# Performance work log

Measured on AMD Instinct MI355X. Metric: run time of the kernel, lower is better.

The kernel has to match this reference:

```python
import jax, jax.numpy as jnp
import numpy as np

C = 256
CK = C // 8  # query/key channels = 32


def setup_inputs() -> dict:
    key = jax.random.key(0)
    ks = jax.random.split(key, 7)
    sc = 0.05
    x = jax.random.normal(ks[0], (4, C, 64, 64), dtype=jnp.float32)
    Wq = jax.random.normal(ks[1], (CK, C), dtype=jnp.float32) * sc
    bq = jax.random.normal(ks[2], (CK,), dtype=jnp.float32) * sc
    Wk = jax.random.normal(ks[3], (CK, C), dtype=jnp.float32) * sc
    bk = jax.random.normal(ks[4], (CK,), dtype=jnp.float32) * sc
    Wv = jax.random.normal(ks[5], (C, C), dtype=jnp.float32) * sc
    bv = jax.random.normal(ks[6], (C,), dtype=jnp.float32) * sc
    gamma = jnp.array([0.5], dtype=jnp.float32)  # nonzero so output/grads are nontrivial
    return {"x": x, "Wq": Wq, "bq": bq, "Wk": Wk, "bk": bk, "Wv": Wv, "bv": bv, "gamma": gamma}


def reference(x, Wq, bq, Wk, bk, Wv, bv, gamma):
    B, Cc, H, W = x.shape
    xf = x.reshape(B, Cc, H * W)  # [B, C, N]
    # 1x1 conv1d == channel-wise matmul
    f = jnp.einsum('kc,bcn->bkn', Wq, xf) + bq[None, :, None]  # [B, CK, N]
    g = jnp.einsum('kc,bcn->bkn', Wk, xf) + bk[None, :, None]  # [B, CK, N]
    h = jnp.einsum('oc,bcn->bon', Wv, xf) + bv[None, :, None]  # [B, C, N]
    # unscaled attention scores: s[b,i,j] = sum_k f[b,k,i] g[b,k,j]
    s = jnp.einsum('bki,bkj->bij', f, g)  # [B, N, N]
    beta = jax.nn.softmax(s, axis=1)      # softmax over query-side axis i (dim=1)
    o = jnp.einsum('bci,bij->bcj', h, beta)  # [B, C, N]
    o = gamma[0] * o
    return o.reshape(B, Cc, H, W)
```

## Files before the change

kernel.cpp:

```cpp
#include <hip/hip_runtime.h>
#include <math.h>

#define BB 4
#define CC 256
#define CKK 32
#define NN 4096
#define TI 32
#define NT (NN / TI)
#define SM_OFF 40.0f

typedef __attribute__((ext_vector_type(8))) short short8v;
typedef __attribute__((ext_vector_type(4))) short short4v;
typedef __attribute__((ext_vector_type(4))) float f32x4;

static __device__ inline unsigned short f2bf(float x) {
    union { float f; unsigned u; } v; v.f = x;
    unsigned r = v.u + 0x7fffu + ((v.u >> 16) & 1u);
    return (unsigned short)(r >> 16);
}
static __device__ inline float bf2f(unsigned short h) {
    union { unsigned u; float f; } v; v.u = ((unsigned)h) << 16;
    return v.f;
}

__global__ __launch_bounds__(256) void prep_w(
    const float* __restrict__ Wq, const float* __restrict__ Wk,
    const float* __restrict__ Wv, unsigned short* __restrict__ Wbf)
{
    int e = blockIdx.x * 256 + threadIdx.x;
    int row = e >> 8, c = e & 255;
    float v;
    if (row < 32)      v = Wq[row * 256 + c];
    else if (row < 64) v = Wk[(row - 32) * 256 + c];
    else               v = Wv[(row - 64) * 256 + c];
    Wbf[e] = f2bf(v);
}

__global__ __launch_bounds__(256, 4) void proj_kernel(
    const float* __restrict__ x,
    const unsigned short* __restrict__ Wbf,
    const float* __restrict__ bq, const float* __restrict__ bk,
    const float* __restrict__ bv,
    unsigned short* __restrict__ fF, unsigned short* __restrict__ gT,
    unsigned short* __restrict__ hF)
{
    __shared__ unsigned short xsh[32 * 264];
    __shared__ unsigned short xsl[32 * 264];

    const int t = threadIdx.x;
    const int b = blockIdx.x >> 7;
    const int n_b = (blockIdx.x & 127) * 32;
    const int lane = t & 63;
    const int wave = t >> 6;
    const int jl = lane & 15;
    const int quad = lane >> 4;

    {
        const int q = t & 7, cb = t >> 3;
        #pragma unroll
        for (int cc = 0; cc < 8; ++cc) {
            int c = cb + cc * 32;
            float4 v = *(const float4*)(x + ((size_t)b * CC + c) * NN + n_b + q * 4);
            float vv[4] = {v.x, v.y, v.z, v.w};
            #pragma unroll
            for (int e = 0; e < 4; ++e) {
                int n = q * 4 + e;
                unsigned short h = f2bf(vv[e]);
                unsigned short l = f2bf(vv[e] - bf2f(h));
                xsh[n * 264 + c] = h;
                xsl[n * 264 + c] = l;
            }
        }
    }
    __syncthreads();

    const int rowbase_w = wave * 80;
    #pragma unroll 1
    for (int nt = 0; nt < 2; ++nt) {
        short8v bhi[8], blo[8];
        #pragma unroll
        for (int k = 0; k < 8; ++k) {
            bhi[k] = *(const short8v*)&xsh[(nt * 16 + jl) * 264 + k * 32 + quad * 8];
            blo[k] = *(const short8v*)&xsl[(nt * 16 + jl) * 264 + k * 32 + quad * 8];
        }
        const int ng = n_b + nt * 16 + jl;
        const int it  = ng >> 5;
        const int il  = ng & 31;
        const int ihh = (ng >> 4) & 1;
        #pragma unroll 1
        for (int mt = 0; mt < 5; ++mt) {
            int rowbase = rowbase_w + mt * 16;
            const unsigned short* wrow = Wbf + (size_t)(rowbase + jl) * CC;
            f32x4 acch = (f32x4){0.f, 0.f, 0.f, 0.f};
            f32x4 accl = (f32x4){0.f, 0.f, 0.f, 0.f};
            #pragma unroll
            for (int k = 0; k < 8; ++k) {
                short8v a = *(const short8v*)(wrow + k * 32 + quad * 8);
                acch = __builtin_amdgcn_mfma_f32_16x16x32_bf16(a, bhi[k], acch, 0, 0, 0);
                accl = __builtin_amdgcn_mfma_f32_16x16x32_bf16(a, blo[k], accl, 0, 0, 0);
            }
            f32x4 acc;
            #pragma unroll
            for (int r = 0; r < 4; ++r) acc[r] = acch[r] + accl[r];
            int rlo = rowbase + quad * 4;
            if (rowbase < 32) {
                float4 bias = *(const float4*)(bq + rlo);
                short4v o;
                o[0] = (short)f2bf(acc[0] + bias.x); o[1] = (short)f2bf(acc[1] + bias.y);
                o[2] = (short)f2bf(acc[2] + bias.z); o[3] = (short)f2bf(acc[3] + bias.w);
                size_t dst = (((size_t)b * NT + it) * 2 + ihh) * 512
                           + (size_t)((rlo >> 3) * 16 + (ng & 15)) * 8 + (rlo & 7);
                *(short4v*)(fF + dst) = o;
            } else if (rowbase < 64) {
                float4 bias = *(const float4*)(bk + rlo - 32);
                short4v o;
                o[0] = (short)f2bf(acc[0] + bias.x); o[1] = (short)f2bf(acc[1] + bias.y);
                o[2] = (short)f2bf(acc[2] + bias.z); o[3] = (short)f2bf(acc[3] + bias.w);
                *(short4v*)(gT + ((size_t)b * NN + ng) * CKK + (rlo - 32)) = o;
            } else {
                const float* bp = bv + rlo - 64;
                #pragma unroll
                for (int r = 0; r < 4; ++r) {
                    int c = rlo - 64 + r;
                    size_t dst = (((size_t)b * NT + it) * 16 + (c >> 4)) * 512
                               + (size_t)((il >> 3) * 16 + (c & 15)) * 8 + (il & 7);
                    hF[dst] = f2bf(acc[r] + bp[r]);
                }
            }
        }
    }
}

__global__ __launch_bounds__(512, 2) void attn_kernel(
    const unsigned short* __restrict__ fF,
    const unsigned short* __restrict__ gT,
    const unsigned short* __restrict__ hF,
    const float* __restrict__ gamma,
    float* __restrict__ out)
{
    __shared__ unsigned short pa[2][4][512];
    __shared__ float ls[8][16];
    __shared__ float ls2[4][16];

    const int t = threadIdx.x;
    const int lane = t & 63;
    const int wave = t >> 6;
    const int bi = blockIdx.x;
    const int b  = bi & 3;
    const int j0 = (bi >> 2) * 64;
    const int jl = lane & 15;
    const int quad = lane >> 4;
    const int jc = wave & 3;
    const int ih = wave >> 2;
    const int c0 = wave * 32;
    const int cg0 = wave * 2;

    const unsigned short* fFb = fF + (size_t)b * NT * 2 * 512;
    const unsigned short* hFb = hF + (size_t)b * NT * 16 * 512;

    short8v bg = *(const short8v*)(gT + ((size_t)b * NN + j0 + jc * 16 + jl) * CKK + quad * 8);

    f32x4 acc[8];
    #pragma unroll
    for (int q = 0; q < 8; ++q) acc[q] = (f32x4){0.f, 0.f, 0.f, 0.f};
    float l_run = 0.f;

    const f32x4 zoff = (f32x4){-SM_OFF, -SM_OFF, -SM_OFF, -SM_OFF};

    const int Lw = ((ih * 2 + (quad >> 1)) * 16 + jl) * 8 + (quad & 1) * 4;

    short8v af0 = *(const short8v*)(fFb + (size_t)(0 * 2 + ih) * 512 + lane * 8);
    short8v ahc0 = *(const short8v*)(hFb + ((size_t)0 * 16 + cg0 + 0) * 512 + lane * 8);
    short8v ahc1 = *(const short8v*)(hFb + ((size_t)0 * 16 + cg0 + 1) * 512 + lane * 8);
    f32x4 s0 = __builtin_amdgcn_mfma_f32_16x16x32_bf16(af0, bg, zoff, 0, 0, 0);
    short8v afn = *(const short8v*)(fFb + (size_t)(1 * 2 + ih) * 512 + lane * 8);
    {
        float e0 = __expf(s0[0]), e1 = __expf(s0[1]);
        float e2 = __expf(s0[2]), e3 = __expf(s0[3]);
        l_run += (e0 + e1) + (e2 + e3);
        unsigned p01, p23;
        asm("v_cvt_pk_bf16_f32 %0, %1, %2" : "=v"(p01) : "v"(e0), "v"(e1));
        asm("v_cvt_pk_bf16_f32 %0, %1, %2" : "=v"(p23) : "v"(e2), "v"(e3));
        uint2 pw; pw.x = p01; pw.y = p23;
        *(uint2*)&pa[0][jc][Lw] = pw;
    }
    asm volatile("s_waitcnt lgkmcnt(0)" ::: "memory");
    __builtin_amdgcn_s_barrier();
    asm volatile("" ::: "memory");

    #pragma unroll 1
    for (int it = 0; it < NT - 1; ++it) {
        const int buf = it & 1;

        f32x4 s = __builtin_amdgcn_mfma_f32_16x16x32_bf16(afn, bg, zoff, 0, 0, 0);

        {
            const int i2 = (it + 2 < NT ? it + 2 : NT - 1);
            afn = *(const short8v*)(fFb + ((size_t)i2 * 2 + ih) * 512 + lane * 8);
        }
        short8v ahn0 = *(const short8v*)(hFb + ((size_t)(it + 1) * 16 + cg0 + 0) * 512 + lane * 8);
        short8v ahn1 = *(const short8v*)(hFb + ((size_t)(it + 1) * 16 + cg0 + 1) * 512 + lane * 8);

        #pragma unroll
        for (int jc2 = 0; jc2 < 4; ++jc2) {
            short8v bp = *(const short8v*)&pa[buf][jc2][lane * 8];
            acc[jc2 * 2 + 0] = __builtin_amdgcn_mfma_f32_16x16x32_bf16(ahc0, bp, acc[jc2 * 2 + 0], 0, 0, 0);
            acc[jc2 * 2 + 1] = __builtin_amdgcn_mfma_f32_16x16x32_bf16(ahc1, bp, acc[jc2 * 2 + 1], 0, 0, 0);
        }

        {
            float e0 = __expf(s[0]), e1 = __expf(s[1]);
            float e2 = __expf(s[2]), e3 = __expf(s[3]);
            l_run += (e0 + e1) + (e2 + e3);
            unsigned p01, p23;
            asm("v_cvt_pk_bf16_f32 %0, %1, %2" : "=v"(p01) : "v"(e0), "v"(e1));
            asm("v_cvt_pk_bf16_f32 %0, %1, %2" : "=v"(p23) : "v"(e2), "v"(e3));
            uint2 pw; pw.x = p01; pw.y = p23;
            *(uint2*)&pa[buf ^ 1][jc][Lw] = pw;
        }

        asm volatile("s_waitcnt lgkmcnt(0)" ::: "memory");
        __builtin_amdgcn_s_barrier();
        asm volatile("" ::: "memory");

        ahc0 = ahn0; ahc1 = ahn1;
    }

    {
        const int buf = (NT - 1) & 1;
        #pragma unroll
        for (int jc2 = 0; jc2 < 4; ++jc2) {
            short8v bp = *(const short8v*)&pa[buf][jc2][lane * 8];
            acc[jc2 * 2 + 0] = __builtin_amdgcn_mfma_f32_16x16x32_bf16(ahc0, bp, acc[jc2 * 2 + 0], 0, 0, 0);
            acc[jc2 * 2 + 1] = __builtin_amdgcn_mfma_f32_16x16x32_bf16(ahc1, bp, acc[jc2 * 2 + 1], 0, 0, 0);
        }
    }

    l_run += __shfl_xor(l_run, 16, 64);
    l_run += __shfl_xor(l_run, 32, 64);
    if (quad == 0) ls[wave][jl] = l_run;
    __syncthreads();
    if (wave < 4 && quad == 0)
        ls2[wave][jl] = gamma[0] / (ls[wave][jl] + ls[wave + 4][jl]);
    __syncthreads();

    #pragma unroll
    for (int jc2 = 0; jc2 < 4; ++jc2) {
        float sc = ls2[jc2][jl];
        #pragma unroll
        for (int cc = 0; cc < 2; ++cc) {
            f32x4 a = acc[jc2 * 2 + cc];
            size_t addr = ((size_t)b * CC + c0 + cc * 16 + quad * 4) * NN + j0 + jc2 * 16 + jl;
            #pragma unroll
            for (int r = 0; r < 4; ++r)
                out[addr + (size_t)r * NN] = a[r] * sc;
        }
    }
}

extern "C" void kernel_launch(void* const* d_in, const int* in_sizes, int n_in,
                              void* d_out, int out_size, void* d_ws, size_t ws_size,
                              hipStream_t stream) {
    const float* x     = (const float*)d_in[0];
    const float* Wq    = (const float*)d_in[1];
    const float* bq    = (const float*)d_in[2];
    const float* Wk    = (const float*)d_in[3];
    const float* bk    = (const float*)d_in[4];
    const float* Wv    = (const float*)d_in[5];
    const float* bv    = (const float*)d_in[6];
    const float* gamma = (const float*)d_in[7];
    float* out = (float*)d_out;

    unsigned short* Wbf = (unsigned short*)d_ws;
    unsigned short* fF  = Wbf + 320 * 256;
    unsigned short* gT  = fF + (size_t)BB * NN * CKK;
    unsigned short* hF  = gT + (size_t)BB * NN * CKK;

    prep_w<<<320, 256, 0, stream>>>(Wq, Wk, Wv, Wbf);
    proj_kernel<<<BB * (NN / 32), 256, 0, stream>>>(x, Wbf, bq, bk, bv, fF, gT, hF);
    attn_kernel<<<BB * (NN / 64), 512, 0, stream>>>(fF, gT, hF, gamma, out);
}
```

Measured before the change: 159.8 us.

## Split PV accumulation by alternating i-tiles across wave halves with LDS reduction

Each wave now owns 64 output channels instead of 32 and handles only every other i-tile for the P·V MFMA, alternating between the two wave halves. Each wave therefore loads four h fragments every other iteration instead of two every iteration. The two partial accumulators are summed through a new LDS buffer before output. Compute-heavy iterations are raised with s_setprio so one half's MFMA work can overlap the other half's exp and softmax work, at the cost of doubled accumulator registers and extra LDS use, which may lower occupancy.

```diff
diff --git a/kernel.cpp b/kernel.cpp
--- a/kernel.cpp
+++ b/kernel.cpp
@@ -139,6 +139,7 @@
     float* __restrict__ out)
 {
     __shared__ unsigned short pa[2][4][512];
+    __shared__ f32x4 eb[4][4][4][64];
     __shared__ float ls[8][16];
     __shared__ float ls2[4][16];
 
@@ -150,30 +151,30 @@
     const int j0 = (bi >> 2) * 64;
     const int jl = lane & 15;
     const int quad = lane >> 4;
-    const int jc = wave & 3;
-    const int ih = wave >> 2;
-    const int c0 = wave * 32;
-    const int cg0 = wave * 2;
+    const int cg  = wave & 3;
+    const int ihw = wave >> 2;
 
     const unsigned short* fFb = fF + (size_t)b * NT * 2 * 512;
     const unsigned short* hFb = hF + (size_t)b * NT * 16 * 512;
 
-    short8v bg = *(const short8v*)(gT + ((size_t)b * NN + j0 + jc * 16 + jl) * CKK + quad * 8);
-
-    f32x4 acc[8];
+    short8v bg = *(const short8v*)(gT + ((size_t)b * NN + j0 + cg * 16 + jl) * CKK + quad * 8);
+
+    f32x4 acc[16];
     #pragma unroll
-    for (int q = 0; q < 8; ++q) acc[q] = (f32x4){0.f, 0.f, 0.f, 0.f};
+    for (int q = 0; q < 16; ++q) acc[q] = (f32x4){0.f, 0.f, 0.f, 0.f};
     float l_run = 0.f;
 
     const f32x4 zoff = (f32x4){-SM_OFF, -SM_OFF, -SM_OFF, -SM_OFF};
 
-    const int Lw = ((ih * 2 + (quad >> 1)) * 16 + jl) * 8 + (quad & 1) * 4;
-
-    short8v af0 = *(const short8v*)(fFb + (size_t)(0 * 2 + ih) * 512 + lane * 8);
-    short8v ahc0 = *(const short8v*)(hFb + ((size_t)0 * 16 + cg0 + 0) * 512 + lane * 8);
-    short8v ahc1 = *(const short8v*)(hFb + ((size_t)0 * 16 + cg0 + 1) * 512 + lane * 8);
+    const int Lw = ((ihw * 2 + (quad >> 1)) * 16 + jl) * 8 + (quad & 1) * 4;
+
+    short8v af0 = *(const short8v*)(fFb + (size_t)(0 * 2 + ihw) * 512 + lane * 8);
+    short8v ah0 = *(const short8v*)(hFb + ((size_t)ihw * 16 + cg * 4 + 0) * 512 + lane * 8);
+    short8v ah1 = *(const short8v*)(hFb + ((size_t)ihw * 16 + cg * 4 + 1) * 512 + lane * 8);
+    short8v ah2 = *(const short8v*)(hFb + ((size_t)ihw * 16 + cg * 4 + 2) * 512 + lane * 8);
+    short8v ah3 = *(const short8v*)(hFb + ((size_t)ihw * 16 + cg * 4 + 3) * 512 + lane * 8);
     f32x4 s0 = __builtin_amdgcn_mfma_f32_16x16x32_bf16(af0, bg, zoff, 0, 0, 0);
-    short8v afn = *(const short8v*)(fFb + (size_t)(1 * 2 + ih) * 512 + lane * 8);
+    short8v afn = *(const short8v*)(fFb + (size_t)(1 * 2 + ihw) * 512 + lane * 8);
     {
         float e0 = __expf(s0[0]), e1 = __expf(s0[1]);
         float e2 = __expf(s0[2]), e3 = __expf(s0[3]);
@@ -182,7 +183,7 @@
         asm("v_cvt_pk_bf16_f32 %0, %1, %2" : "=v"(p01) : "v"(e0), "v"(e1));
         asm("v_cvt_pk_bf16_f32 %0, %1, %2" : "=v"(p23) : "v"(e2), "v"(e3));
         uint2 pw; pw.x = p01; pw.y = p23;
-        *(uint2*)&pa[0][jc][Lw] = pw;
+        *(uint2*)&pa[0][cg][Lw] = pw;
     }
     asm volatile("s_waitcnt lgkmcnt(0)" ::: "memory");
     __builtin_amdgcn_s_barrier();
@@ -193,19 +194,30 @@
         const int buf = it & 1;
 
         f32x4 s = __builtin_amdgcn_mfma_f32_16x16x32_bf16(afn, bg, zoff, 0, 0, 0);
-
         {
-            const int i2 = (it + 2 < NT ? it + 2 : NT - 1);
-            afn = *(const short8v*)(fFb + ((size_t)i2 * 2 + ih) * 512 + lane * 8);
-        }
-        short8v ahn0 = *(const short8v*)(hFb + ((size_t)(it + 1) * 16 + cg0 + 0) * 512 + lane * 8);
-        short8v ahn1 = *(const short8v*)(hFb + ((size_t)(it + 1) * 16 + cg0 + 1) * 512 + lane * 8);
-
-        #pragma unroll
-        for (int jc2 = 0; jc2 < 4; ++jc2) {
-            short8v bp = *(const short8v*)&pa[buf][jc2][lane * 8];
-            acc[jc2 * 2 + 0] = __builtin_amdgcn_mfma_f32_16x16x32_bf16(ahc0, bp, acc[jc2 * 2 + 0], 0, 0, 0);
-            acc[jc2 * 2 + 1] = __builtin_amdgcn_mfma_f32_16x16x32_bf16(ahc1, bp, acc[jc2 * 2 + 1], 0, 0, 0);
+            const int i2f = (it + 2 < NT ? it + 2 : NT - 1);
+            afn = *(const short8v*)(fFb + ((size_t)i2f * 2 + ihw) * 512 + lane * 8);
+        }
+
+        const bool on = ((it & 1) == ihw);
+        short8v an0, an1, an2, an3;
+        if (on) {
+            const int i2 = (it + 2 <= NT - 2 + ihw) ? it + 2 : it;
+            an0 = *(const short8v*)(hFb + ((size_t)i2 * 16 + cg * 4 + 0) * 512 + lane * 8);
+            an1 = *(const short8v*)(hFb + ((size_t)i2 * 16 + cg * 4 + 1) * 512 + lane * 8);
+            an2 = *(const short8v*)(hFb + ((size_t)i2 * 16 + cg * 4 + 2) * 512 + lane * 8);
+            an3 = *(const short8v*)(hFb + ((size_t)i2 * 16 + cg * 4 + 3) * 512 + lane * 8);
+
+            __builtin_amdgcn_s_setprio(1);
+            #pragma unroll
+            for (int jc2 = 0; jc2 < 4; ++jc2) {
+                short8v bp = *(const short8v*)&pa[buf][jc2][lane * 8];
+                acc[jc2 * 4 + 0] = __builtin_amdgcn_mfma_f32_16x16x32_bf16(ah0, bp, acc[jc2 * 4 + 0], 0, 0, 0);
+                acc[jc2 * 4 + 1] = __builtin_amdgcn_mfma_f32_16x16x32_bf16(ah1, bp, acc[jc2 * 4 + 1], 0, 0, 0);
+                acc[jc2 * 4 + 2] = __builtin_amdgcn_mfma_f32_16x16x32_bf16(ah2, bp, acc[jc2 * 4 + 2], 0, 0, 0);
+                acc[jc2 * 4 + 3] = __builtin_amdgcn_mfma_f32_16x16x32_bf16(ah3, bp, acc[jc2 * 4 + 3], 0, 0, 0);
+            }
+            __builtin_amdgcn_s_setprio(0);
         }
 
         {
@@ -216,41 +228,53 @@
             asm("v_cvt_pk_bf16_f32 %0, %1, %2" : "=v"(p01) : "v"(e0), "v"(e1));
             asm("v_cvt_pk_bf16_f32 %0, %1, %2" : "=v"(p23) : "v"(e2), "v"(e3));
             uint2 pw; pw.x = p01; pw.y = p23;
-            *(uint2*)&pa[buf ^ 1][jc][Lw] = pw;
+            *(uint2*)&pa[buf ^ 1][cg][Lw] = pw;
         }
 
         asm volatile("s_waitcnt lgkmcnt(0)" ::: "memory");
         __builtin_amdgcn_s_barrier();
         asm volatile("" ::: "memory");
 
-        ahc0 = ahn0; ahc1 = ahn1;
-    }
-
-    {
+        if (on) { ah0 = an0; ah1 = an1; ah2 = an2; ah3 = an3; }
+    }
+
+    if (ihw == 1) {
         const int buf = (NT - 1) & 1;
         #pragma unroll
         for (int jc2 = 0; jc2 < 4; ++jc2) {
             short8v bp = *(const short8v*)&pa[buf][jc2][lane * 8];
-            acc[jc2 * 2 + 0] = __builtin_amdgcn_mfma_f32_16x16x32_bf16(ahc0, bp, acc[jc2 * 2 + 0], 0, 0, 0);
-            acc[jc2 * 2 + 1] = __builtin_amdgcn_mfma_f32_16x16x32_bf16(ahc1, bp, acc[jc2 * 2 + 1], 0, 0, 0);
+            acc[jc2 * 4 + 0] = __builtin_amdgcn_mfma_f32_16x16x32_bf16(ah0, bp, acc[jc2 * 4 + 0], 0, 0, 0);
+            acc[jc2 * 4 + 1] = __builtin_amdgcn_mfma_f32_16x16x32_bf16(ah1, bp, acc[jc2 * 4 + 1], 0, 0, 0);
+            acc[jc2 * 4 + 2] = __builtin_amdgcn_mfma_f32_16x16x32_bf16(ah2, bp, acc[jc2 * 4 + 2], 0, 0, 0);
+            acc[jc2 * 4 + 3] = __builtin_amdgcn_mfma_f32_16x16x32_bf16(ah3, bp, acc[jc2 * 4 + 3], 0, 0, 0);
         }
     }
 
     l_run += __shfl_xor(l_run, 16, 64);
     l_run += __shfl_xor(l_run, 32, 64);
     if (quad == 0) ls[wave][jl] = l_run;
+
+    const int jw = (1 - ihw) * 2;
+    #pragma unroll
+    for (int m = 0; m < 2; ++m)
+        #pragma unroll
+        for (int cc = 0; cc < 4; ++cc)
+            eb[cg][jw + m][cc][lane] = acc[(jw + m) * 4 + cc];
     __syncthreads();
+
     if (wave < 4 && quad == 0)
         ls2[wave][jl] = gamma[0] / (ls[wave][jl] + ls[wave + 4][jl]);
     __syncthreads();
 
+    const int jr = ihw * 2;
     #pragma unroll
-    for (int jc2 = 0; jc2 < 4; ++jc2) {
+    for (int m = 0; m < 2; ++m) {
+        const int jc2 = jr + m;
         float sc = ls2[jc2][jl];
         #pragma unroll
-        for (int cc = 0; cc < 2; ++cc) {
-            f32x4 a = acc[jc2 * 2 + cc];
-            size_t addr = ((size_t)b * CC + c0 + cc * 16 + quad * 4) * NN + j0 + jc2 * 16 + jl;
+        for (int cc = 0; cc < 4; ++cc) {
+            f32x4 a = acc[jc2 * 4 + cc] + eb[cg][jc2][cc][lane];
+            size_t addr = ((size_t)b * CC + cg * 64 + cc * 16 + quad * 4) * NN + j0 + jc2 * 16 + jl;
             #pragma unroll
             for (int r = 0; r < 4; ++r)
                 out[addr + (size_t)r * NN] = a[r] * sc;
```

New measurement: 324.1 us. 2.03x slower.

## Process two query tiles per barrier iteration and raise MFMA wave priority

Applied to the files above, without the earlier changes.

The attention main loop now handles two 32-row query tiles per iteration, with a doubled shared-memory P buffer. This halves the number of block-wide barriers and deepens prefetch of f and h fragments. The PV MFMA section is also wrapped in s_setprio to favour matrix work over the exp phase of other waves. In exchange, register pressure and LDS use go up, which could hurt occupancy at 2 blocks per CU.

```diff
diff --git a/kernel.cpp b/kernel.cpp
--- a/kernel.cpp
+++ b/kernel.cpp
@@ -138,7 +138,7 @@
     const float* __restrict__ gamma,
     float* __restrict__ out)
 {
-    __shared__ unsigned short pa[2][4][512];
+    __shared__ unsigned short pa[2][2][4][512];
     __shared__ float ls[8][16];
     __shared__ float ls2[4][16];
 
@@ -152,7 +152,6 @@
     const int quad = lane >> 4;
     const int jc = wave & 3;
     const int ih = wave >> 2;
-    const int c0 = wave * 32;
     const int cg0 = wave * 2;
 
     const unsigned short* fFb = fF + (size_t)b * NT * 2 * 512;
@@ -169,70 +168,107 @@
 
     const int Lw = ((ih * 2 + (quad >> 1)) * 16 + jl) * 8 + (quad & 1) * 4;
 
-    short8v af0 = *(const short8v*)(fFb + (size_t)(0 * 2 + ih) * 512 + lane * 8);
-    short8v ahc0 = *(const short8v*)(hFb + ((size_t)0 * 16 + cg0 + 0) * 512 + lane * 8);
-    short8v ahc1 = *(const short8v*)(hFb + ((size_t)0 * 16 + cg0 + 1) * 512 + lane * 8);
-    f32x4 s0 = __builtin_amdgcn_mfma_f32_16x16x32_bf16(af0, bg, zoff, 0, 0, 0);
-    short8v afn = *(const short8v*)(fFb + (size_t)(1 * 2 + ih) * 512 + lane * 8);
+    short8v afA = *(const short8v*)(fFb + (size_t)(0 * 2 + ih) * 512 + lane * 8);
+    short8v afB = *(const short8v*)(fFb + (size_t)(1 * 2 + ih) * 512 + lane * 8);
+    short8v ahA0 = *(const short8v*)(hFb + ((size_t)0 * 16 + cg0 + 0) * 512 + lane * 8);
+    short8v ahA1 = *(const short8v*)(hFb + ((size_t)0 * 16 + cg0 + 1) * 512 + lane * 8);
+    short8v ahB0 = *(const short8v*)(hFb + ((size_t)1 * 16 + cg0 + 0) * 512 + lane * 8);
+    short8v ahB1 = *(const short8v*)(hFb + ((size_t)1 * 16 + cg0 + 1) * 512 + lane * 8);
+    f32x4 s0A = __builtin_amdgcn_mfma_f32_16x16x32_bf16(afA, bg, zoff, 0, 0, 0);
+    f32x4 s0B = __builtin_amdgcn_mfma_f32_16x16x32_bf16(afB, bg, zoff, 0, 0, 0);
+    afA = *(const short8v*)(fFb + (size_t)(2 * 2 + ih) * 512 + lane * 8);
+    afB = *(const short8v*)(fFb + (size_t)(3 * 2 + ih) * 512 + lane * 8);
     {
-        float e0 = __expf(s0[0]), e1 = __expf(s0[1]);
-        float e2 = __expf(s0[2]), e3 = __expf(s0[3]);
-        l_run += (e0 + e1) + (e2 + e3);
-        unsigned p01, p23;
+        float e0 = __expf(s0A[0]), e1 = __expf(s0A[1]);
+        float e2 = __expf(s0A[2]), e3 = __expf(s0A[3]);
+        float f0 = __expf(s0B[0]), f1 = __expf(s0B[1]);
+        float f2 = __expf(s0B[2]), f3 = __expf(s0B[3]);
+        l_run += ((e0 + e1) + (e2 + e3)) + ((f0 + f1) + (f2 + f3));
+        unsigned p01, p23, q01, q23;
         asm("v_cvt_pk_bf16_f32 %0, %1, %2" : "=v"(p01) : "v"(e0), "v"(e1));
         asm("v_cvt_pk_bf16_f32 %0, %1, %2" : "=v"(p23) : "v"(e2), "v"(e3));
+        asm("v_cvt_pk_bf16_f32 %0, %1, %2" : "=v"(q01) : "v"(f0), "v"(f1));
+        asm("v_cvt_pk_bf16_f32 %0, %1, %2" : "=v"(q23) : "v"(f2), "v"(f3));
         uint2 pw; pw.x = p01; pw.y = p23;
-        *(uint2*)&pa[0][jc][Lw] = pw;
+        uint2 qw; qw.x = q01; qw.y = q23;
+        *(uint2*)&pa[0][0][jc][Lw] = pw;
+        *(uint2*)&pa[0][1][jc][Lw] = qw;
     }
     asm volatile("s_waitcnt lgkmcnt(0)" ::: "memory");
     __builtin_amdgcn_s_barrier();
     asm volatile("" ::: "memory");
 
     #pragma unroll 1
-    for (int it = 0; it < NT - 1; ++it) {
-        const int buf = it & 1;
-
-        f32x4 s = __builtin_amdgcn_mfma_f32_16x16x32_bf16(afn, bg, zoff, 0, 0, 0);
+    for (int it2 = 0; it2 < NT / 2 - 1; ++it2) {
+        const int buf = it2 & 1;
+        const int tn = 2 * it2 + 2;
+
+        f32x4 sA = __builtin_amdgcn_mfma_f32_16x16x32_bf16(afA, bg, zoff, 0, 0, 0);
+        f32x4 sB = __builtin_amdgcn_mfma_f32_16x16x32_bf16(afB, bg, zoff, 0, 0, 0);
 
         {
-            const int i2 = (it + 2 < NT ? it + 2 : NT - 1);
-            afn = *(const short8v*)(fFb + ((size_t)i2 * 2 + ih) * 512 + lane * 8);
-        }
-        short8v ahn0 = *(const short8v*)(hFb + ((size_t)(it + 1) * 16 + cg0 + 0) * 512 + lane * 8);
-        short8v ahn1 = *(const short8v*)(hFb + ((size_t)(it + 1) * 16 + cg0 + 1) * 512 + lane * 8);
-
+            const int i4 = (tn + 2 < NT ? tn + 2 : NT - 1);
+            const int i5 = (tn + 3 < NT ? tn + 3 : NT - 1);
+            afA = *(const short8v*)(fFb + ((size_t)i4 * 2 + ih) * 512 + lane * 8);
+            afB = *(const short8v*)(fFb + ((size_t)i5 * 2 + ih) * 512 + lane * 8);
+        }
+        short8v anA0 = *(const short8v*)(hFb + ((size_t)tn * 16 + cg0 + 0) * 512 + lane * 8);
+        short8v anA1 = *(const short8v*)(hFb + ((size_t)tn * 16 + cg0 + 1) * 512 + lane * 8);
+        short8v anB0 = *(const short8v*)(hFb + ((size_t)(tn + 1) * 16 + cg0 + 0) * 512 + lane * 8);
+        short8v anB1 = *(const short8v*)(hFb + ((size_t)(tn + 1) * 16 + cg0 + 1) * 512 + lane * 8);
+
+        __builtin_amdgcn_s_setprio(1);
         #pragma unroll
         for (int jc2 = 0; jc2 < 4; ++jc2) {
-            short8v bp = *(const short8v*)&pa[buf][jc2][lane * 8];
-            acc[jc2 * 2 + 0] = __builtin_amdgcn_mfma_f32_16x16x32_bf16(ahc0, bp, acc[jc2 * 2 + 0], 0, 0, 0);
-            acc[jc2 * 2 + 1] = __builtin_amdgcn_mfma_f32_16x16x32_bf16(ahc1, bp, acc[jc2 * 2 + 1], 0, 0, 0);
-        }
+            short8v bpA = *(const short8v*)&pa[buf][0][jc2][lane * 8];
+            acc[jc2 * 2 + 0] = __builtin_amdgcn_mfma_f32_16x16x32_bf16(ahA0, bpA, acc[jc2 * 2 + 0], 0, 0, 0);
+            acc[jc2 * 2 + 1] = __builtin_amdgcn_mfma_f32_16x16x32_bf16(ahA1, bpA, acc[jc2 * 2 + 1], 0, 0, 0);
+        }
+        #pragma unroll
+        for (int jc2 = 0; jc2 < 4; ++jc2) {
+            short8v bpB = *(const short8v*)&pa[buf][1][jc2][lane * 8];
+            acc[jc2 * 2 + 0] = __builtin_amdgcn_mfma_f32_16x16x32_bf16(ahB0, bpB, acc[jc2 * 2 + 0], 0, 0, 0);
+            acc[jc2 * 2 + 1] = __builtin_amdgcn_mfma_f32_16x16x32_bf16(ahB1, bpB, acc[jc2 * 2 + 1], 0, 0, 0);
+        }
+        __builtin_amdgcn_s_setprio(0);
 
         {
-            float e0 = __expf(s[0]), e1 = __expf(s[1]);
-            float e2 = __expf(s[2]), e3 = __expf(s[3]);
-            l_run += (e0 + e1) + (e2 + e3);
-            unsigned p01, p23;
+            float e0 = __expf(sA[0]), e1 = __expf(sA[1]);
+            float e2 = __expf(sA[2]), e3 = __expf(sA[3]);
+            float f0 = __expf(sB[0]), f1 = __expf(sB[1]);
+            float f2 = __expf(sB[2]), f3 = __expf(sB[3]);
+            l_run += ((e0 + e1) + (e2 + e3)) + ((f0 + f1) + (f2 + f3));
+            unsigned p01, p23, q01, q23;
             asm("v_cvt_pk_bf16_f32 %0, %1, %2" : "=v"(p01) : "v"(e0), "v"(e1));
             asm("v_cvt_pk_bf16_f32 %0, %1, %2" : "=v"(p23) : "v"(e2), "v"(e3));
+            asm("v_cvt_pk_bf16_f32 %0, %1, %2" : "=v"(q01) : "v"(f0), "v"(f1));
+            asm("v_cvt_pk_bf16_f32 %0, %1, %2" : "=v"(q23) : "v"(f2), "v"(f3));
             uint2 pw; pw.x = p01; pw.y = p23;
-            *(uint2*)&pa[buf ^ 1][jc][Lw] = pw;
+            uint2 qw; qw.x = q01; qw.y = q23;
+            *(uint2*)&pa[buf ^ 1][0][jc][Lw] = pw;
+            *(uint2*)&pa[buf ^ 1][1][jc][Lw] = qw;
         }
 
         asm volatile("s_waitcnt lgkmcnt(0)" ::: "memory");
         __builtin_amdgcn_s_barrier();
         asm volatile("" ::: "memory");
 
-        ahc0 = ahn0; ahc1 = ahn1;
+        ahA0 = anA0; ahA1 = anA1; ahB0 = anB0; ahB1 = anB1;
     }
 
     {
-        const int buf = (NT - 1) & 1;
+        const int buf = (NT / 2 - 1) & 1;
         #pragma unroll
         for (int jc2 = 0; jc2 < 4; ++jc2) {
-            short8v bp = *(const short8v*)&pa[buf][jc2][lane * 8];
-            acc[jc2 * 2 + 0] = __builtin_amdgcn_mfma_f32_16x16x32_bf16(ahc0, bp, acc[jc2 * 2 + 0], 0, 0, 0);
-            acc[jc2 * 2 + 1] = __builtin_amdgcn_mfma_f32_16x16x32_bf16(ahc1, bp, acc[jc2 * 2 + 1], 0, 0, 0);
+            short8v bpA = *(const short8v*)&pa[buf][0][jc2][lane * 8];
+            acc[jc2 * 2 + 0] = __builtin_amdgcn_mfma_f32_16x16x32_bf16(ahA0, bpA, acc[jc2 * 2 + 0], 0, 0, 0);
+            acc[jc2 * 2 + 1] = __builtin_amdgcn_mfma_f32_16x16x32_bf16(ahA1, bpA, acc[jc2 * 2 + 1], 0, 0, 0);
+        }
+        #pragma unroll
+        for (int jc2 = 0; jc2 < 4; ++jc2) {
+            short8v bpB = *(const short8v*)&pa[buf][1][jc2][lane * 8];
+            acc[jc2 * 2 + 0] = __builtin_amdgcn_mfma_f32_16x16x32_bf16(ahB0, bpB, acc[jc2 * 2 + 0], 0, 0, 0);
+            acc[jc2 * 2 + 1] = __builtin_amdgcn_mfma_f32_16x16x32_bf16(ahB1, bpB, acc[jc2 * 2 + 1], 0, 0, 0);
         }
     }
 
@@ -250,7 +286,7 @@
         #pragma unroll
         for (int cc = 0; cc < 2; ++cc) {
             f32x4 a = acc[jc2 * 2 + cc];
-            size_t addr = ((size_t)b * CC + c0 + cc * 16 + quad * 4) * NN + j0 + jc2 * 16 + jl;
+            size_t addr = ((size_t)b * CC + wave * 32 + cc * 16 + quad * 4) * NN + j0 + jc2 * 16 + jl;
             #pragma unroll
             for (int r = 0; r < 4; ++r)
                 out[addr + (size_t)r * NN] = a[r] * sc;
```

Result: faster. 154.5 us (-3.3%).

## Use 16-wave attention blocks processing two i-tiles per step with shared f staging

Applied to the files above, without the earlier changes.

The attention kernel goes from 8 waves to 16 waves per block. Each wave now owns 16 output channels and works on two i-tiles per iteration, which halves the serial loop trip count. Four waves stage f tiles through LDS so that global loads of f are shared, and MFMA sections get raised priority via s_setprio. The weight prep kernel also writes Wbf in MFMA fragment order so that the projection kernel reads coalesced 16-byte lanes. The larger block and 4-blocks-per-CU launch bound add register pressure and barrier cost across more waves.

```diff
diff --git a/kernel.cpp b/kernel.cpp
--- a/kernel.cpp
+++ b/kernel.cpp
@@ -7,6 +7,7 @@
 #define NN 4096
 #define TI 32
 #define NT (NN / TI)
+#define NP (NT / 2)
 #define SM_OFF 40.0f
 
 typedef __attribute__((ext_vector_type(8))) short short8v;
@@ -27,13 +28,19 @@
     const float* __restrict__ Wq, const float* __restrict__ Wk,
     const float* __restrict__ Wv, unsigned short* __restrict__ Wbf)
 {
-    int e = blockIdx.x * 256 + threadIdx.x;
-    int row = e >> 8, c = e & 255;
+    int o = blockIdx.x * 256 + threadIdx.x;
+    int rb   = o >> 12;
+    int rem  = o & 4095;
+    int k    = rem >> 9;
+    int lane = (rem >> 3) & 63;
+    int e    = rem & 7;
+    int row  = rb * 16 + (lane & 15);
+    int c    = k * 32 + (lane >> 4) * 8 + e;
     float v;
     if (row < 32)      v = Wq[row * 256 + c];
     else if (row < 64) v = Wk[(row - 32) * 256 + c];
     else               v = Wv[(row - 64) * 256 + c];
-    Wbf[e] = f2bf(v);
+    Wbf[o] = f2bf(v);
 }
 
 __global__ __launch_bounds__(256, 4) void proj_kernel(
@@ -90,12 +97,13 @@
         #pragma unroll 1
         for (int mt = 0; mt < 5; ++mt) {
             int rowbase = rowbase_w + mt * 16;
-            const unsigned short* wrow = Wbf + (size_t)(rowbase + jl) * CC;
+            const int rb = rowbase >> 4;
+            const unsigned short* wf = Wbf + (size_t)rb * 8 * 512;
             f32x4 acch = (f32x4){0.f, 0.f, 0.f, 0.f};
             f32x4 accl = (f32x4){0.f, 0.f, 0.f, 0.f};
             #pragma unroll
             for (int k = 0; k < 8; ++k) {
-                short8v a = *(const short8v*)(wrow + k * 32 + quad * 8);
+                short8v a = *(const short8v*)(wf + (size_t)k * 512 + lane * 8);
                 acch = __builtin_amdgcn_mfma_f32_16x16x32_bf16(a, bhi[k], acch, 0, 0, 0);
                 accl = __builtin_amdgcn_mfma_f32_16x16x32_bf16(a, blo[k], accl, 0, 0, 0);
             }
@@ -131,15 +139,16 @@
     }
 }
 
-__global__ __launch_bounds__(512, 2) void attn_kernel(
+__global__ __launch_bounds__(1024, 4) void attn_kernel(
     const unsigned short* __restrict__ fF,
     const unsigned short* __restrict__ gT,
     const unsigned short* __restrict__ hF,
     const float* __restrict__ gamma,
     float* __restrict__ out)
 {
-    __shared__ unsigned short pa[2][4][512];
-    __shared__ float ls[8][16];
+    __shared__ unsigned short pa[2][2][4][512];
+    __shared__ unsigned short fsh[2][4][512];
+    __shared__ float ls[16][16];
     __shared__ float ls2[4][16];
 
     const int t = threadIdx.x;
@@ -150,30 +159,35 @@
     const int j0 = (bi >> 2) * 64;
     const int jl = lane & 15;
     const int quad = lane >> 4;
-    const int jc = wave & 3;
-    const int ih = wave >> 2;
-    const int c0 = wave * 32;
-    const int cg0 = wave * 2;
+    const int jcq  = wave & 3;
+    const int ihq  = (wave >> 2) & 1;
+    const int subq = wave >> 3;
+    const int cg   = wave;
+    const int fsid = subq * 2 + ihq;
 
     const unsigned short* fFb = fF + (size_t)b * NT * 2 * 512;
     const unsigned short* hFb = hF + (size_t)b * NT * 16 * 512;
 
-    short8v bg = *(const short8v*)(gT + ((size_t)b * NN + j0 + jc * 16 + jl) * CKK + quad * 8);
-
-    f32x4 acc[8];
+    short8v bg = *(const short8v*)(gT + ((size_t)b * NN + j0 + jcq * 16 + jl) * CKK + quad * 8);
+
+    f32x4 acc[4];
     #pragma unroll
-    for (int q = 0; q < 8; ++q) acc[q] = (f32x4){0.f, 0.f, 0.f, 0.f};
+    for (int q = 0; q < 4; ++q) acc[q] = (f32x4){0.f, 0.f, 0.f, 0.f};
     float l_run = 0.f;
 
     const f32x4 zoff = (f32x4){-SM_OFF, -SM_OFF, -SM_OFF, -SM_OFF};
 
-    const int Lw = ((ih * 2 + (quad >> 1)) * 16 + jl) * 8 + (quad & 1) * 4;
-
-    short8v af0 = *(const short8v*)(fFb + (size_t)(0 * 2 + ih) * 512 + lane * 8);
-    short8v ahc0 = *(const short8v*)(hFb + ((size_t)0 * 16 + cg0 + 0) * 512 + lane * 8);
-    short8v ahc1 = *(const short8v*)(hFb + ((size_t)0 * 16 + cg0 + 1) * 512 + lane * 8);
+    const int Lw = ((ihq * 2 + (quad >> 1)) * 16 + jl) * 8 + (quad & 1) * 4;
+
+    short8v af0 = *(const short8v*)(fFb + ((size_t)subq * 2 + ihq) * 512 + lane * 8);
+    short8v ah0 = *(const short8v*)(hFb + ((size_t)0 * 16 + cg) * 512 + lane * 8);
+    short8v ah1 = *(const short8v*)(hFb + ((size_t)1 * 16 + cg) * 512 + lane * 8);
+    short8v an0 = *(const short8v*)(hFb + ((size_t)2 * 16 + cg) * 512 + lane * 8);
+    short8v an1 = *(const short8v*)(hFb + ((size_t)3 * 16 + cg) * 512 + lane * 8);
+    short8v fs0;
+    if (wave < 4)
+        fs0 = *(const short8v*)(fFb + ((size_t)(2 + (wave >> 1)) * 2 + (wave & 1)) * 512 + lane * 8);
     f32x4 s0 = __builtin_amdgcn_mfma_f32_16x16x32_bf16(af0, bg, zoff, 0, 0, 0);
-    short8v afn = *(const short8v*)(fFb + (size_t)(1 * 2 + ih) * 512 + lane * 8);
     {
         float e0 = __expf(s0[0]), e1 = __expf(s0[1]);
         float e2 = __expf(s0[2]), e3 = __expf(s0[3]);
@@ -182,31 +196,40 @@
         asm("v_cvt_pk_bf16_f32 %0, %1, %2" : "=v"(p01) : "v"(e0), "v"(e1));
         asm("v_cvt_pk_bf16_f32 %0, %1, %2" : "=v"(p23) : "v"(e2), "v"(e3));
         uint2 pw; pw.x = p01; pw.y = p23;
-        *(uint2*)&pa[0][jc][Lw] = pw;
-    }
+        *(uint2*)&pa[0][subq][jcq][Lw] = pw;
+    }
+    if (wave < 4)
+        *(short8v*)&fsh[1][wave][lane * 8] = fs0;
     asm volatile("s_waitcnt lgkmcnt(0)" ::: "memory");
     __builtin_amdgcn_s_barrier();
     asm volatile("" ::: "memory");
 
     #pragma unroll 1
-    for (int it = 0; it < NT - 1; ++it) {
-        const int buf = it & 1;
-
-        f32x4 s = __builtin_amdgcn_mfma_f32_16x16x32_bf16(afn, bg, zoff, 0, 0, 0);
-
-        {
-            const int i2 = (it + 2 < NT ? it + 2 : NT - 1);
-            afn = *(const short8v*)(fFb + ((size_t)i2 * 2 + ih) * 512 + lane * 8);
-        }
-        short8v ahn0 = *(const short8v*)(hFb + ((size_t)(it + 1) * 16 + cg0 + 0) * 512 + lane * 8);
-        short8v ahn1 = *(const short8v*)(hFb + ((size_t)(it + 1) * 16 + cg0 + 1) * 512 + lane * 8);
-
+    for (int p = 0; p < NP - 1; ++p) {
+        const int buf = p & 1;
+
+        short8v af = *(const short8v*)&fsh[buf ^ 1][fsid][lane * 8];
+        f32x4 s = __builtin_amdgcn_mfma_f32_16x16x32_bf16(af, bg, zoff, 0, 0, 0);
+
+        short8v fs2;
+        if (wave < 4) {
+            const int tp2 = (p + 2 < NP ? p + 2 : NP - 1);
+            fs2 = *(const short8v*)(fFb + ((size_t)(2 * tp2 + (wave >> 1)) * 2 + (wave & 1)) * 512 + lane * 8);
+        }
+
+        const int pq = (p + 2 < NP ? p + 2 : NP - 1);
+        short8v aq0 = *(const short8v*)(hFb + ((size_t)(2 * pq) * 16 + cg) * 512 + lane * 8);
+        short8v aq1 = *(const short8v*)(hFb + ((size_t)(2 * pq + 1) * 16 + cg) * 512 + lane * 8);
+
+        __builtin_amdgcn_s_setprio(1);
         #pragma unroll
         for (int jc2 = 0; jc2 < 4; ++jc2) {
-            short8v bp = *(const short8v*)&pa[buf][jc2][lane * 8];
-            acc[jc2 * 2 + 0] = __builtin_amdgcn_mfma_f32_16x16x32_bf16(ahc0, bp, acc[jc2 * 2 + 0], 0, 0, 0);
-            acc[jc2 * 2 + 1] = __builtin_amdgcn_mfma_f32_16x16x32_bf16(ahc1, bp, acc[jc2 * 2 + 1], 0, 0, 0);
-        }
+            short8v bpA = *(const short8v*)&pa[buf][0][jc2][lane * 8];
+            acc[jc2] = __builtin_amdgcn_mfma_f32_16x16x32_bf16(ah0, bpA, acc[jc2], 0, 0, 0);
+            short8v bpB = *(const short8v*)&pa[buf][1][jc2][lane * 8];
+            acc[jc2] = __builtin_amdgcn_mfma_f32_16x16x32_bf16(ah1, bpB, acc[jc2], 0, 0, 0);
+        }
+        __builtin_amdgcn_s_setprio(0);
 
         {
             float e0 = __expf(s[0]), e1 = __expf(s[1]);
@@ -216,23 +239,26 @@
             asm("v_cvt_pk_bf16_f32 %0, %1, %2" : "=v"(p01) : "v"(e0), "v"(e1));
             asm("v_cvt_pk_bf16_f32 %0, %1, %2" : "=v"(p23) : "v"(e2), "v"(e3));
             uint2 pw; pw.x = p01; pw.y = p23;
-            *(uint2*)&pa[buf ^ 1][jc][Lw] = pw;
-        }
+            *(uint2*)&pa[buf ^ 1][subq][jcq][Lw] = pw;
+        }
+        if (wave < 4)
+            *(short8v*)&fsh[buf][wave][lane * 8] = fs2;
 
         asm volatile("s_waitcnt lgkmcnt(0)" ::: "memory");
         __builtin_amdgcn_s_barrier();
         asm volatile("" ::: "memory");
 
-        ahc0 = ahn0; ahc1 = ahn1;
+        ah0 = an0; ah1 = an1; an0 = aq0; an1 = aq1;
     }
 
     {
-        const int buf = (NT - 1) & 1;
+        const int buf = (NP - 1) & 1;
         #pragma unroll
         for (int jc2 = 0; jc2 < 4; ++jc2) {
-            short8v bp = *(const short8v*)&pa[buf][jc2][lane * 8];
-            acc[jc2 * 2 + 0] = __builtin_amdgcn_mfma_f32_16x16x32_bf16(ahc0, bp, acc[jc2 * 2 + 0], 0, 0, 0);
-            acc[jc2 * 2 + 1] = __builtin_amdgcn_mfma_f32_16x16x32_bf16(ahc1, bp, acc[jc2 * 2 + 1], 0, 0, 0);
+            short8v bpA = *(const short8v*)&pa[buf][0][jc2][lane * 8];
+            acc[jc2] = __builtin_amdgcn_mfma_f32_16x16x32_bf16(ah0, bpA, acc[jc2], 0, 0, 0);
+            short8v bpB = *(const short8v*)&pa[buf][1][jc2][lane * 8];
+            acc[jc2] = __builtin_amdgcn_mfma_f32_16x16x32_bf16(ah1, bpB, acc[jc2], 0, 0, 0);
         }
     }
 
@@ -241,20 +267,18 @@
     if (quad == 0) ls[wave][jl] = l_run;
     __syncthreads();
     if (wave < 4 && quad == 0)
-        ls2[wave][jl] = gamma[0] / (ls[wave][jl] + ls[wave + 4][jl]);
+        ls2[wave][jl] = gamma[0] / (((ls[wave][jl] + ls[wave + 4][jl])
+                                   + (ls[wave + 8][jl] + ls[wave + 12][jl])));
     __syncthreads();
 
     #pragma unroll
     for (int jc2 = 0; jc2 < 4; ++jc2) {
         float sc = ls2[jc2][jl];
-        #pragma unroll
-        for (int cc = 0; cc < 2; ++cc) {
-            f32x4 a = acc[jc2 * 2 + cc];
-            size_t addr = ((size_t)b * CC + c0 + cc * 16 + quad * 4) * NN + j0 + jc2 * 16 + jl;
-            #pragma unroll
-            for (int r = 0; r < 4; ++r)
-                out[addr + (size_t)r * NN] = a[r] * sc;
-        }
+        f32x4 a = acc[jc2];
+        size_t addr = ((size_t)b * CC + cg * 16 + quad * 4) * NN + j0 + jc2 * 16 + jl;
+        #pragma unroll
+        for (int r = 0; r < 4; ++r)
+            out[addr + (size_t)r * NN] = a[r] * sc;
     }
 }
 
@@ -278,5 +302,5 @@
 
     prep_w<<<320, 256, 0, stream>>>(Wq, Wk, Wv, Wbf);
     proj_kernel<<<BB * (NN / 32), 256, 0, stream>>>(x, Wbf, bq, bk, bv, fF, gT, hF);
-    attn_kernel<<<BB * (NN / 64), 512, 0, stream>>>(fF, gT, hF, gamma, out);
-}
+    attn_kernel<<<BB * (NN / 64), 1024, 0, stream>>>(fF, gT, hF, gamma, out);
+}
```

Result: faster. 142.6 us (-10.8%).
